# Optimization experiments

Hardware: AMD Instinct MI355X
Metric: run time of the kernel (lower is better)

The kernel has to match this reference:

```python
import jax, jax.numpy as jnp
import numpy as np

V, E, T_MAX, H, L = 20000, 384, 512, 8, 8
D = E // H  # head size 48
FF = 4 * E


def setup_inputs() -> dict:
    key = jax.random.key(0)
    ks = jax.random.split(key, 24)
    B, T = 16, 512
    s = 0.02
    return {
        "index": jax.random.randint(ks[0], (B, T), 0, V, dtype=jnp.int64),
        "targets": jax.random.randint(ks[1], (B, T), 0, V, dtype=jnp.int64),
        "tok_emb": s * jax.random.normal(ks[2], (V, E), jnp.float32),
        "pos_emb": s * jax.random.normal(ks[3], (T_MAX, E), jnp.float32),
        "Wq": s * jax.random.normal(ks[4], (L, E, H, D), jnp.float32),
        "bq": jnp.zeros((L, H, D), jnp.float32),
        "Wk": s * jax.random.normal(ks[5], (L, E, H, D), jnp.float32),
        "bk": jnp.zeros((L, H, D), jnp.float32),
        "Wv": s * jax.random.normal(ks[6], (L, E, H, D), jnp.float32),
        "bv": jnp.zeros((L, H, D), jnp.float32),
        "Wo": s * jax.random.normal(ks[7], (L, E, E), jnp.float32),
        "bo": jnp.zeros((L, E), jnp.float32),
        "ln1_g": jnp.ones((L, E), jnp.float32),
        "ln1_b": jnp.zeros((L, E), jnp.float32),
        "ln2_g": jnp.ones((L, E), jnp.float32),
        "ln2_b": jnp.zeros((L, E), jnp.float32),
        "W1": s * jax.random.normal(ks[8], (L, E, FF), jnp.float32),
        "b1": jnp.zeros((L, FF), jnp.float32),
        "W2": s * jax.random.normal(ks[9], (L, FF, E), jnp.float32),
        "b2": jnp.zeros((L, E), jnp.float32),
        "lnf_g": jnp.ones((E,), jnp.float32),
        "lnf_b": jnp.zeros((E,), jnp.float32),
        "lm_b": jnp.zeros((V,), jnp.float32),
    }


def layernorm(x, g, b, eps=1e-5):
    mu = jnp.mean(x, axis=-1, keepdims=True)
    var = jnp.var(x, axis=-1, keepdims=True)
    return (x - mu) * jax.lax.rsqrt(var + eps) * g + b


def reference(index, targets, tok_emb, pos_emb, Wq, bq, Wk, bk, Wv, bv, Wo, bo,
              ln1_g, ln1_b, ln2_g, ln2_b, W1, b1, W2, b2, lnf_g, lnf_b, lm_b):
    B, T = index.shape
    x = tok_emb[index] + pos_emb[:T]  # [B,T,E]
    causal = jnp.tril(jnp.ones((T, T), bool))
    scale = D ** -0.5
    for l in range(L):
        h = layernorm(x, ln1_g[l], ln1_b[l])
        q = jnp.einsum('bte,ehd->bthd', h, Wq[l]) + bq[l]
        k = jnp.einsum('bte,ehd->bthd', h, Wk[l]) + bk[l]
        v = jnp.einsum('bte,ehd->bthd', h, Wv[l]) + bv[l]
        scores = jnp.einsum('bqhd,bkhd->bhqk', q, k) * scale
        scores = jnp.where(causal, scores, -jnp.inf)
        w = jax.nn.softmax(scores, axis=-1)
        attn = jnp.einsum('bhqk,bkhd->bqhd', w, v).reshape(B, T, E)
        x = x + attn @ Wo[l] + bo[l]
        h2 = layernorm(x, ln2_g[l], ln2_b[l])
        ff = jax.nn.gelu(h2 @ W1[l] + b1[l], approximate=False) @ W2[l] + b2[l]
        x = x + ff
    x = layernorm(x, lnf_g, lnf_b)
    logits = x @ tok_emb.T + lm_b  # tied weights
    logits = logits.reshape(B * T, V)
    logp = jax.nn.log_softmax(logits, axis=-1)
    loss = -jnp.mean(jnp.take_along_axis(logp, targets.reshape(-1, 1), axis=-1))
    return logits, loss
```

## Files before the change

### kernel.cpp

```cpp
#include <hip/hip_runtime.h>
#include <hip/hip_bf16.h>
#include <math.h>

#define M_ROWS 8192
#define E_DIM 384
#define FF_DIM 1536
#define V_DIM 20000
#define VPAD 20096
#define N_LAYER 8
#define QK_SCALE 0.14433756729740643f
#define PSTRIDE 320
#define NPART 314

typedef __bf16 bf16x8 __attribute__((ext_vector_type(8)));
typedef short  s16x8  __attribute__((ext_vector_type(8)));
typedef float  f32x4  __attribute__((ext_vector_type(4)));
typedef __hip_bfloat16 bf16_t;

__device__ __forceinline__ void gl2lds16(const void* g, void* l) {
    __builtin_amdgcn_global_load_lds((const __attribute__((address_space(1))) void*)g,
                                     (__attribute__((address_space(3))) void*)l, 16, 0, 0);
}
__device__ __forceinline__ unsigned short bf16bits(float v) {
    return __builtin_bit_cast(unsigned short, __float2bfloat16(v));
}

__global__ __launch_bounds__(256) void tconv_kernel(
    const float* __restrict__ in, bf16_t* __restrict__ out,
    int K, int N, int outRows, int rowoff)
{
    __shared__ float tile[32][33];
    const int n0 = blockIdx.x * 32, k0 = blockIdx.y * 32;
    const float* ip = in + (size_t)blockIdx.z * K * N;
    bf16_t* op = out + (size_t)blockIdx.z * outRows * K;
    const int tx = threadIdx.x & 31, ty = threadIdx.x >> 5;
#pragma unroll
    for (int i = 0; i < 32; i += 8)
        tile[ty + i][tx] = ip[(size_t)(k0 + ty + i) * N + n0 + tx];
    __syncthreads();
#pragma unroll
    for (int i = 0; i < 32; i += 8)
        op[(size_t)(rowoff + n0 + ty + i) * K + k0 + tx] = __float2bfloat16(tile[tx][ty + i]);
}

__global__ __launch_bounds__(256) void tokconv_kernel(
    const float* __restrict__ tok, bf16_t* __restrict__ out)
{
    const int total = VPAD * 48;
    for (int idx = blockIdx.x * 256 + threadIdx.x; idx < total; idx += gridDim.x * 256) {
        int row = idx / 48, gc = idx - row * 48;
        int col = gc * 8;
        s16x8 pk = {};
        if (row < V_DIM) {
            const float* tp = tok + (size_t)row * E_DIM + col;
            float4 f0 = *(const float4*)tp;
            float4 f1 = *(const float4*)(tp + 4);
            pk[0] = (short)bf16bits(f0.x); pk[1] = (short)bf16bits(f0.y);
            pk[2] = (short)bf16bits(f0.z); pk[3] = (short)bf16bits(f0.w);
            pk[4] = (short)bf16bits(f1.x); pk[5] = (short)bf16bits(f1.y);
            pk[6] = (short)bf16bits(f1.z); pk[7] = (short)bf16bits(f1.w);
        }
        *(s16x8*)&out[(size_t)row * E_DIM + col] = pk;
    }
}

__global__ __launch_bounds__(256) void bqkv_kernel(
    const float* __restrict__ bq, const float* __restrict__ bk,
    const float* __restrict__ bv, float* __restrict__ o)
{
    int i = blockIdx.x * 256 + threadIdx.x;
    if (i < N_LAYER * 1152) {
        int l = i / 1152, c = i - l * 1152;
        float v = (c < 384) ? bq[l * 384 + c] : (c < 768) ? bk[l * 384 + c - 384] : bv[l * 384 + c - 768];
        o[i] = v;
    }
}

__global__ __launch_bounds__(256) void embed_kernel(
    const int* __restrict__ idx, const float* __restrict__ tok,
    const float* __restrict__ pos, float* __restrict__ x)
{
    int row = blockIdx.x * 4 + (threadIdx.x >> 6);
    int lane = threadIdx.x & 63;
    int t = row & 511;
    int id = idx[row];
    const float* tr = tok + (size_t)id * E_DIM;
    const float* pr = pos + (size_t)t * E_DIM;
    float* xr = x + (size_t)row * E_DIM;
#pragma unroll
    for (int i = 0; i < 6; i++) { int c = lane + i * 64; xr[c] = tr[c] + pr[c]; }
}

__global__ __launch_bounds__(256) void ln_kernel(
    const float* __restrict__ x, const float* __restrict__ g,
    const float* __restrict__ b, bf16_t* __restrict__ out)
{
    int row = blockIdx.x * 4 + (threadIdx.x >> 6);
    int lane = threadIdx.x & 63;
    const float* xr = x + (size_t)row * E_DIM;
    float vals[6];
    float s = 0.f;
#pragma unroll
    for (int i = 0; i < 6; i++) { vals[i] = xr[lane + i * 64]; s += vals[i]; }
#pragma unroll
    for (int off = 1; off < 64; off <<= 1) s += __shfl_xor(s, off);
    float mu = s * (1.f / E_DIM);
    float sq = 0.f;
#pragma unroll
    for (int i = 0; i < 6; i++) { float d = vals[i] - mu; sq += d * d; }
#pragma unroll
    for (int off = 1; off < 64; off <<= 1) sq += __shfl_xor(sq, off);
    float rstd = rsqrtf(sq * (1.f / E_DIM) + 1e-5f);
    bf16_t* orow = out + (size_t)row * E_DIM;
#pragma unroll
    for (int i = 0; i < 6; i++) {
        int c = lane + i * 64;
        orow[c] = __float2bfloat16((vals[i] - mu) * rstd * g[c] + b[c]);
    }
}

template <int MODE, int MREP>
__global__ __launch_bounds__(256) void gemm_kernel(
    const bf16_t* __restrict__ A, const bf16_t* __restrict__ Bt,
    const float* __restrict__ bias, void* __restrict__ Cv, void* __restrict__ C2,
    int Ncols, int K)
{
    constexpr int BMR = MREP * 32;
    constexpr int ASH = BMR * 32;
    constexpr int BUFSH = ASH + 4096;
    constexpr int NLD = MREP / 2 + 2;
    __shared__ __align__(16) short smem[3 * BUFSH];
    const int t = threadIdx.x;
    const int w = t >> 6, lane = t & 63;
    const int wm = w >> 1, wn = w & 1;
    const int bm = (MODE == 3 ? blockIdx.x : blockIdx.y) * BMR;
    const int bn = (MODE == 3 ? blockIdx.y : blockIdx.x) * 128;

    f32x4 acc[MREP][4];
#pragma unroll
    for (int m = 0; m < MREP; m++)
#pragma unroll
        for (int n = 0; n < 4; n++)
            acc[m][n] = (f32x4){0.f, 0.f, 0.f, 0.f};

    const int lg = lane >> 4;
    const int ll = lane & 15;
    const int nt = K / 32;

    auto stagef = [&](int kt, int buf) {
        short* sA = smem + buf * BUFSH;
        short* sB = sA + ASH;
#pragma unroll
        for (int i = 0; i < MREP / 2; i++) {
            int li = i * 256 + t;
            int g = li >> (MREP == 4 ? 7 : 6);
            int row = li & (BMR - 1);
            gl2lds16(A + (size_t)(bm + row) * K + kt + g * 8,
                     sA + (size_t)(i * 256 + w * 64) * 8);
        }
#pragma unroll
        for (int i = 0; i < 2; i++) {
            int li = i * 256 + t;
            gl2lds16(Bt + (size_t)(bn + (li & 127)) * K + kt + (li >> 7) * 8,
                     sB + (size_t)(i * 256 + w * 64) * 8);
        }
    };

    stagef(0, 0);
    stagef(32, 1);

    for (int tt = 0; tt < nt; ++tt) {
        if (tt + 2 < nt) {
            stagef((tt + 2) * 32, (tt + 2) % 3);
            asm volatile("s_waitcnt vmcnt(%0)" :: "n"(2 * NLD) : "memory");
        } else if (tt + 1 < nt) {
            asm volatile("s_waitcnt vmcnt(%0)" :: "n"(NLD) : "memory");
        } else {
            asm volatile("s_waitcnt vmcnt(0)" ::: "memory");
        }
        __builtin_amdgcn_s_barrier();

        const short* sA = smem + (tt % 3) * BUFSH;
        const short* sB = sA + ASH;
        bf16x8 af[MREP], bfr[4];
#pragma unroll
        for (int m = 0; m < MREP; m++)
            af[m] = __builtin_bit_cast(bf16x8,
                *(const s16x8*)&sA[(lg * BMR + wm * (BMR / 2) + m * 16 + ll) * 8]);
#pragma unroll
        for (int n = 0; n < 4; n++)
            bfr[n] = __builtin_bit_cast(bf16x8,
                *(const s16x8*)&sB[(lg * 128 + wn * 64 + n * 16 + ll) * 8]);
#pragma unroll
        for (int m = 0; m < MREP; m++)
#pragma unroll
            for (int n = 0; n < 4; n++)
                acc[m][n] = __builtin_amdgcn_mfma_f32_16x16x32_bf16(bfr[n], af[m], acc[m][n], 0, 0, 0);

        __builtin_amdgcn_s_barrier();
    }

    const int rowm0 = bm + wm * (BMR / 2) + ll;
    const int coln0 = bn + wn * 64 + lg * 4;

    if constexpr (MODE == 4) {
        if (bn < 768) {
            bf16_t* qkvb = (bf16_t*)Cv;
            const float sc = (bn >= 384) ? 1.f : QK_SCALE;
#pragma unroll
            for (int n = 0; n < 4; n++) {
                const int coln = coln0 + n * 16;
                const float4 b4 = *(const float4*)&bias[coln];
#pragma unroll
                for (int m = 0; m < MREP; m++) {
                    const int row = rowm0 + m * 16;
                    ushort4 pk;
                    pk.x = bf16bits((acc[m][n][0] + b4.x) * sc);
                    pk.y = bf16bits((acc[m][n][1] + b4.y) * sc);
                    pk.z = bf16bits((acc[m][n][2] + b4.z) * sc);
                    pk.w = bf16bits((acc[m][n][3] + b4.w) * sc);
                    *(ushort4*)&qkvb[(size_t)row * 1152 + coln] = pk;
                }
            }
        } else {
            bf16_t* vtb = (bf16_t*)C2;
            const int cc0 = coln0 - 768;
#pragma unroll
            for (int n = 0; n < 4; n++) {
                const float4 b4 = *(const float4*)&bias[coln0 + n * 16];
#pragma unroll
                for (int m = 0; m < MREP; m++) {
                    const int row = rowm0 + m * 16;
                    const int bb = row >> 9, tt2 = row & 511;
                    bf16_t* vb = vtb + (size_t)bb * 384 * 512 + tt2;
                    vb[(size_t)(cc0 + n * 16 + 0) * 512] = __float2bfloat16(acc[m][n][0] + b4.x);
                    vb[(size_t)(cc0 + n * 16 + 1) * 512] = __float2bfloat16(acc[m][n][1] + b4.y);
                    vb[(size_t)(cc0 + n * 16 + 2) * 512] = __float2bfloat16(acc[m][n][2] + b4.z);
                    vb[(size_t)(cc0 + n * 16 + 3) * 512] = __float2bfloat16(acc[m][n][3] + b4.w);
                }
            }
        }
    } else if constexpr (MODE == 1) {
        float* C = (float*)Cv;
#pragma unroll
        for (int n = 0; n < 4; n++) {
            const int coln = coln0 + n * 16;
            const float4 b4 = *(const float4*)&bias[coln];
#pragma unroll
            for (int m = 0; m < MREP; m++) {
                const int row = rowm0 + m * 16;
                float4 cv = *(float4*)&C[(size_t)row * Ncols + coln];
                cv.x += acc[m][n][0] + b4.x;
                cv.y += acc[m][n][1] + b4.y;
                cv.z += acc[m][n][2] + b4.z;
                cv.w += acc[m][n][3] + b4.w;
                *(float4*)&C[(size_t)row * Ncols + coln] = cv;
            }
        }
    } else if constexpr (MODE == 2) {
        bf16_t* O = (bf16_t*)Cv;
#pragma unroll
        for (int n = 0; n < 4; n++) {
            const int coln = coln0 + n * 16;
            const float4 b4 = *(const float4*)&bias[coln];
#pragma unroll
            for (int m = 0; m < MREP; m++) {
                const int row = rowm0 + m * 16;
                float v0 = acc[m][n][0] + b4.x, v1 = acc[m][n][1] + b4.y;
                float v2 = acc[m][n][2] + b4.z, v3 = acc[m][n][3] + b4.w;
                v0 = 0.5f * v0 * (1.f + erff(v0 * 0.70710678118654752f));
                v1 = 0.5f * v1 * (1.f + erff(v1 * 0.70710678118654752f));
                v2 = 0.5f * v2 * (1.f + erff(v2 * 0.70710678118654752f));
                v3 = 0.5f * v3 * (1.f + erff(v3 * 0.70710678118654752f));
                ushort4 pk;
                pk.x = bf16bits(v0); pk.y = bf16bits(v1);
                pk.z = bf16bits(v2); pk.w = bf16bits(v3);
                *(ushort4*)&O[(size_t)row * Ncols + coln] = pk;
            }
        }
    } else if constexpr (MODE == 3) {
        float* C = (float*)Cv;
        float* pbuf = (float*)C2;
        const int ptile = blockIdx.y * 2 + wn;
#pragma unroll
        for (int m = 0; m < MREP; m++) {
            const int row = rowm0 + m * 16;
            float se = 0.f;
#pragma unroll
            for (int n = 0; n < 4; n++) {
                const int coln = coln0 + n * 16;
                if (coln + 3 < Ncols) {
                    const float4 b4 = *(const float4*)&bias[coln];
                    f32x4 v;
                    v[0] = acc[m][n][0] + b4.x;
                    v[1] = acc[m][n][1] + b4.y;
                    v[2] = acc[m][n][2] + b4.z;
                    v[3] = acc[m][n][3] + b4.w;
                    __builtin_nontemporal_store(v, (f32x4*)&C[(size_t)row * Ncols + coln]);
                    se += __expf(v[0]) + __expf(v[1]) + __expf(v[2]) + __expf(v[3]);
                } else {
#pragma unroll
                    for (int e = 0; e < 4; e++) {
                        int col = coln + e;
                        if (col < Ncols) {
                            float v = acc[m][n][e] + bias[col];
                            __builtin_nontemporal_store(v, &C[(size_t)row * Ncols + col]);
                            se += __expf(v);
                        }
                    }
                }
            }
            se += __shfl_xor(se, 16);
            se += __shfl_xor(se, 32);
            if (lg == 0)
                __builtin_nontemporal_store(se, &pbuf[(size_t)row * PSTRIDE + ptile]);
        }
    }
}

__global__ __launch_bounds__(256) void attn_kernel(
    const bf16_t* __restrict__ qkvb, const bf16_t* __restrict__ vt,
    bf16_t* __restrict__ o)
{
    const int bh = blockIdx.y;
    const int b = bh >> 3, h = bh & 7;
    __shared__ unsigned short psm[4608];
    const int tid = threadIdx.x;
    const int w = tid >> 6, lane = tid & 63;
    const int ll = lane & 15, g = lane >> 4;

    const bf16_t* kptr = qkvb + (size_t)b * 512 * 1152 + 384 + h * 48;
    const bf16_t* vptr = vt + (size_t)b * 384 * 512 + (size_t)h * 48 * 512;

    auto runQ = [&](int qt) {
        const int q0 = qt * 64;
        const int q_abs = q0 + ll * 4 + w;

        const bf16_t* qrow = qkvb + (size_t)(b * 512 + q_abs) * 1152 + h * 48;
        bf16x8 qf0 = __builtin_bit_cast(bf16x8, *(const s16x8*)(qrow + g * 8));
        bf16x8 qf1 = {};
        if (g < 2) qf1 = __builtin_bit_cast(bf16x8, *(const s16x8*)(qrow + 32 + g * 8));

        f32x4 oacc[3];
#pragma unroll
        for (int df = 0; df < 3; df++) oacc[df] = (f32x4){0.f, 0.f, 0.f, 0.f};
        float ssum = 0.f;
        const int ntiles = 2 * (qt + 1);

        auto loadK = [&](int kbase, bf16x8& c00, bf16x8& c01, bf16x8& c10, bf16x8& c11) {
            const bf16_t* kr0 = kptr + (size_t)(kbase + ll) * 1152;
            const bf16_t* kr1 = kptr + (size_t)(kbase + 16 + ll) * 1152;
            c00 = __builtin_bit_cast(bf16x8, *(const s16x8*)(kr0 + g * 8));
            c10 = __builtin_bit_cast(bf16x8, *(const s16x8*)(kr1 + g * 8));
            bf16x8 z = {};
            c01 = (g < 2) ? __builtin_bit_cast(bf16x8, *(const s16x8*)(kr0 + 32 + g * 8)) : z;
            c11 = (g < 2) ? __builtin_bit_cast(bf16x8, *(const s16x8*)(kr1 + 32 + g * 8)) : z;
        };

        auto doTile = [&](int kbase, int parity,
                          const bf16x8& c00, const bf16x8& c01, const bf16x8& c10, const bf16x8& c11,
                          bool pf, int nbase,
                          bf16x8& n00, bf16x8& n01, bf16x8& n10, bf16x8& n11) {
            bf16x8 vf[3];
#pragma unroll
            for (int df = 0; df < 3; df++)
                vf[df] = __builtin_bit_cast(bf16x8,
                    *(const s16x8*)(vptr + (size_t)(df * 16 + ll) * 512 + kbase + g * 8));
            if (pf) loadK(nbase, n00, n01, n10, n11);

            f32x4 sfr[2];
            {
                f32x4 z0 = {0.f, 0.f, 0.f, 0.f};
                z0 = __builtin_amdgcn_mfma_f32_16x16x32_bf16(c00, qf0, z0, 0, 0, 0);
                z0 = __builtin_amdgcn_mfma_f32_16x16x32_bf16(c01, qf1, z0, 0, 0, 0);
                sfr[0] = z0;
                f32x4 z1 = {0.f, 0.f, 0.f, 0.f};
                z1 = __builtin_amdgcn_mfma_f32_16x16x32_bf16(c10, qf0, z1, 0, 0, 0);
                z1 = __builtin_amdgcn_mfma_f32_16x16x32_bf16(c11, qf1, z1, 0, 0, 0);
                sfr[1] = z1;
            }

            float p[8];
#pragma unroll
            for (int f = 0; f < 2; f++)
#pragma unroll
                for (int j = 0; j < 4; j++) {
                    int key = kbase + f * 16 + g * 4 + j;
                    float sv = sfr[f][j];
                    sv = (key > q_abs) ? -1e30f : sv;
                    float pv = __expf(fminf(sv, 20.f));
                    p[f * 4 + j] = pv;
                    ssum += pv;
                }

            const int pbase = (w * 2 + parity) * 576;
#pragma unroll
            for (int f = 0; f < 2; f++)
#pragma unroll
                for (int j = 0; j < 4; j++)
                    psm[pbase + (f * 16 + g * 4 + j) * 18 + ll] = bf16bits(p[f * 4 + j]);
            s16x8 pr;
#pragma unroll
            for (int i = 0; i < 8; i++)
                pr[i] = (short)psm[pbase + (g * 8 + i) * 18 + ll];
            bf16x8 pfr = __builtin_bit_cast(bf16x8, pr);
#pragma unroll
            for (int df = 0; df < 3; df++)
                oacc[df] = __builtin_amdgcn_mfma_f32_16x16x32_bf16(vf[df], pfr, oacc[df], 0, 0, 0);
        };

        bf16x8 kA0, kA1, kA2, kA3, kB0, kB1, kB2, kB3;
        loadK(0, kA0, kA1, kA2, kA3);
        for (int kt = 0; kt < ntiles; kt += 2) {
            doTile(kt * 32, 0, kA0, kA1, kA2, kA3,
                   true, (kt + 1) * 32, kB0, kB1, kB2, kB3);
            doTile((kt + 1) * 32, 1, kB0, kB1, kB2, kB3,
                   (kt + 2) < ntiles, (kt + 2) * 32, kA0, kA1, kA2, kA3);
        }

        ssum += __shfl_xor(ssum, 16);
        ssum += __shfl_xor(ssum, 32);
        float inv = 1.f / ssum;
        bf16_t* orow = o + (size_t)(b * 512 + q_abs) * 384 + h * 48;
#pragma unroll
        for (int df = 0; df < 3; df++) {
            ushort4 pk;
            pk.x = bf16bits(oacc[df][0] * inv);
            pk.y = bf16bits(oacc[df][1] * inv);
            pk.z = bf16bits(oacc[df][2] * inv);
            pk.w = bf16bits(oacc[df][3] * inv);
            *(ushort4*)&orow[df * 16 + g * 4] = pk;
        }
    };

    runQ(blockIdx.x);
    runQ(7 - blockIdx.x);
}

__global__ __launch_bounds__(256) void loss_row2_kernel(
    const float* __restrict__ pbuf, const float* __restrict__ logits,
    const int* __restrict__ targets, float* __restrict__ rowloss)
{
    int row = blockIdx.x * 4 + (threadIdx.x >> 6);
    int lane = threadIdx.x & 63;
    const float* pr = pbuf + (size_t)row * PSTRIDE;
    float s = 0.f;
    for (int i = lane; i < NPART; i += 64) s += pr[i];
#pragma unroll
    for (int off = 1; off < 64; off <<= 1) s += __shfl_xor(s, off);
    if (lane == 0) {
        int tgt = targets[row];
        rowloss[row] = logf(s) - logits[(size_t)row * V_DIM + tgt];
    }
}

__global__ __launch_bounds__(256) void loss_reduce_kernel(
    const float* __restrict__ rowloss, float* __restrict__ out)
{
    int t = threadIdx.x;
    __shared__ float red[4];
    float s = 0.f;
    for (int i = t; i < M_ROWS; i += 256) s += rowloss[i];
#pragma unroll
    for (int off = 1; off < 64; off <<= 1) s += __shfl_xor(s, off);
    if ((t & 63) == 0) red[t >> 6] = s;
    __syncthreads();
    if (t == 0) out[0] = (red[0] + red[1] + red[2] + red[3]) * (1.f / M_ROWS);
}

extern "C" void kernel_launch(void* const* d_in, const int* in_sizes, int n_in,
                              void* d_out, int out_size, void* d_ws, size_t ws_size,
                              hipStream_t stream)
{
    const int*   index   = (const int*)d_in[0];
    const int*   targets = (const int*)d_in[1];
    const float* tok_emb = (const float*)d_in[2];
    const float* pos_emb = (const float*)d_in[3];
    const float* Wq = (const float*)d_in[4];
    const float* bq = (const float*)d_in[5];
    const float* Wk = (const float*)d_in[6];
    const float* bk = (const float*)d_in[7];
    const float* Wv = (const float*)d_in[8];
    const float* bv = (const float*)d_in[9];
    const float* Wo = (const float*)d_in[10];
    const float* bo = (const float*)d_in[11];
    const float* ln1_g = (const float*)d_in[12];
    const float* ln1_b = (const float*)d_in[13];
    const float* ln2_g = (const float*)d_in[14];
    const float* ln2_b = (const float*)d_in[15];
    const float* W1 = (const float*)d_in[16];
    const float* b1 = (const float*)d_in[17];
    const float* W2 = (const float*)d_in[18];
    const float* b2 = (const float*)d_in[19];
    const float* lnf_g = (const float*)d_in[20];
    const float* lnf_b = (const float*)d_in[21];
    const float* lm_b  = (const float*)d_in[22];

    float* out = (float*)d_out;
    char* wsb = (char*)d_ws;

    float*  x     = (float*)(wsb + 0);
    bf16_t* hbuf  = (bf16_t*)(wsb + 12582912);
    bf16_t* obuf  = (bf16_t*)(wsb + 18874368);
    bf16_t* qkvb  = (bf16_t*)(wsb + 25165824);
    bf16_t* vtb   = (bf16_t*)(wsb + 44040192);
    bf16_t* ffmid = (bf16_t*)(wsb + 18874368);
    float*  pbuf  = (float*)(wsb + 25165824);
    bf16_t* tokb  = (bf16_t*)(wsb + 50331648);
    bf16_t* qkvw  = (bf16_t*)(wsb + 65765376);
    bf16_t* wo_t  = (bf16_t*)(wsb + 72843264);
    bf16_t* w1_t  = (bf16_t*)(wsb + 75202560);
    bf16_t* w2_t  = (bf16_t*)(wsb + 84639744);
    float*  bqkv  = (float*)(wsb + 94076928);
    float*  rowloss = (float*)(wsb + 94113792);

    tokconv_kernel<<<2048, 256, 0, stream>>>(tok_emb, tokb);
    tconv_kernel<<<dim3(12, 12, 8), 256, 0, stream>>>(Wq, qkvw, 384, 384, 1152, 0);
    tconv_kernel<<<dim3(12, 12, 8), 256, 0, stream>>>(Wk, qkvw, 384, 384, 1152, 384);
    tconv_kernel<<<dim3(12, 12, 8), 256, 0, stream>>>(Wv, qkvw, 384, 384, 1152, 768);
    tconv_kernel<<<dim3(12, 12, 8), 256, 0, stream>>>(Wo, wo_t, 384, 384, 384, 0);
    tconv_kernel<<<dim3(48, 12, 8), 256, 0, stream>>>(W1, w1_t, 384, 1536, 1536, 0);
    tconv_kernel<<<dim3(12, 48, 8), 256, 0, stream>>>(W2, w2_t, 1536, 384, 384, 0);
    bqkv_kernel<<<36, 256, 0, stream>>>(bq, bk, bv, bqkv);

    embed_kernel<<<2048, 256, 0, stream>>>(index, tok_emb, pos_emb, x);

    for (int l = 0; l < N_LAYER; l++) {
        const bf16_t* qkvw_l = qkvw + (size_t)l * 1152 * 384;
        const float*  bqkv_l = bqkv + l * 1152;
        ln_kernel<<<2048, 256, 0, stream>>>(x, ln1_g + l * E_DIM, ln1_b + l * E_DIM, hbuf);
        gemm_kernel<4, 4><<<dim3(9, 64), 256, 0, stream>>>(
            hbuf, qkvw_l, bqkv_l, qkvb, vtb, 1152, 384);
        attn_kernel<<<dim3(4, 128), 256, 0, stream>>>(qkvb, vtb, obuf);
        gemm_kernel<1, 2><<<dim3(3, 128), 256, 0, stream>>>(
            obuf, wo_t + (size_t)l * 384 * 384, bo + l * E_DIM, x, nullptr, 384, 384);
        ln_kernel<<<2048, 256, 0, stream>>>(x, ln2_g + l * E_DIM, ln2_b + l * E_DIM, hbuf);
        gemm_kernel<2, 4><<<dim3(12, 64), 256, 0, stream>>>(
            hbuf, w1_t + (size_t)l * 1536 * 384, b1 + l * FF_DIM, ffmid, nullptr, 1536, 384);
        gemm_kernel<1, 2><<<dim3(3, 128), 256, 0, stream>>>(
            ffmid, w2_t + (size_t)l * 384 * 1536, b2 + l * E_DIM, x, nullptr, 384, 1536);
    }

    ln_kernel<<<2048, 256, 0, stream>>>(x, lnf_g, lnf_b, hbuf);
    gemm_kernel<3, 4><<<dim3(64, 157), 256, 0, stream>>>(
        hbuf, tokb, lm_b, out, pbuf, V_DIM, 384);

    loss_row2_kernel<<<2048, 256, 0, stream>>>(pbuf, out, targets, rowloss);
    loss_reduce_kernel<<<1, 256, 0, stream>>>(rowloss, out + (size_t)M_ROWS * V_DIM);
}
```

Before: 1.684 ms.

## Add dedicated logits kernel with register-resident A rows and streamed vocab tiles

Replaces the generic MODE 3 GEMM for the LM head with a persistent-style kernel. Each block keeps its 128 rows of normalized activations in registers for the full K=384 and loops over a range of 128-wide vocab tiles, triple-buffering only the B tiles in LDS. The grid shrinks from 64x157 to 64x8 blocks, and partial sum-exp entries drop to one per 128-column tile. This is meant to cut repeated A loads and per-block launch overhead for the logits GEMM, at the cost of heavy register use (24 bf16x8 A fragments plus 16 accumulators) and only 512 blocks, which may limit occupancy and latency hiding.

Result: faster. 1.641 ms (median of 2 runs) (-2.6%).

```diff
diff --git a/kernel.cpp b/kernel.cpp
--- a/kernel.cpp
+++ b/kernel.cpp
@@ -9,8 +9,8 @@
 #define VPAD 20096
 #define N_LAYER 8
 #define QK_SCALE 0.14433756729740643f
-#define PSTRIDE 320
-#define NPART 314
+#define PSTRIDE 160
+#define NPART 157
 
 typedef __bf16 bf16x8 __attribute__((ext_vector_type(8)));
 typedef short  s16x8  __attribute__((ext_vector_type(8)));
@@ -133,8 +133,8 @@
     const int t = threadIdx.x;
     const int w = t >> 6, lane = t & 63;
     const int wm = w >> 1, wn = w & 1;
-    const int bm = (MODE == 3 ? blockIdx.x : blockIdx.y) * BMR;
-    const int bn = (MODE == 3 ? blockIdx.y : blockIdx.x) * 128;
+    const int bm = blockIdx.y * BMR;
+    const int bn = blockIdx.x * 128;
 
     f32x4 acc[MREP][4];
 #pragma unroll
@@ -278,33 +278,108 @@
                 *(ushort4*)&O[(size_t)row * Ncols + coln] = pk;
             }
         }
-    } else if constexpr (MODE == 3) {
-        float* C = (float*)Cv;
-        float* pbuf = (float*)C2;
-        const int ptile = blockIdx.y * 2 + wn;
-#pragma unroll
-        for (int m = 0; m < MREP; m++) {
-            const int row = rowm0 + m * 16;
+    }
+}
+
+__global__ __launch_bounds__(256) void logits_kernel(
+    const bf16_t* __restrict__ A, const bf16_t* __restrict__ Bt,
+    const float* __restrict__ bias, float* __restrict__ C,
+    float* __restrict__ pbuf)
+{
+    __shared__ __align__(16) short smem[3 * 4096];
+    const int t = threadIdx.x;
+    const int w = t >> 6, lane = t & 63;
+    const int lg = lane >> 4, ll = lane & 15;
+    const int bm = blockIdx.x * 128;
+    const int wr = bm + w * 32;
+    const int tstart = (blockIdx.y * 157) >> 3;
+    const int tend = ((blockIdx.y + 1) * 157) >> 3;
+
+    bf16x8 af[12][2];
+#pragma unroll
+    for (int kt = 0; kt < 12; kt++)
+#pragma unroll
+        for (int m = 0; m < 2; m++)
+            af[kt][m] = __builtin_bit_cast(bf16x8,
+                *(const s16x8*)(A + (size_t)(wr + m * 16 + ll) * E_DIM + kt * 32 + lg * 8));
+
+    auto stageB = [&](int tile, int kt, int buf) {
+        short* sB = smem + buf * 4096;
+#pragma unroll
+        for (int i = 0; i < 2; i++) {
+            int li = i * 256 + t;
+            gl2lds16(Bt + (size_t)(tile * 128 + (li & 127)) * E_DIM + kt * 32 + (li >> 7) * 8,
+                     sB + (size_t)(i * 256 + w * 64) * 8);
+        }
+    };
+
+    stageB(tstart, 0, 0);
+    stageB(tstart, 1, 1);
+
+    for (int tile = tstart; tile < tend; ++tile) {
+        f32x4 acc[2][8];
+#pragma unroll
+        for (int m = 0; m < 2; m++)
+#pragma unroll
+            for (int n = 0; n < 8; n++)
+                acc[m][n] = (f32x4){0.f, 0.f, 0.f, 0.f};
+
+#pragma unroll
+        for (int kt = 0; kt < 12; ++kt) {
+            const int sleft = (tend - 1 - tile) * 12 + (11 - kt);
+            if (kt + 2 < 12) {
+                stageB(tile, kt + 2, (kt + 2) % 3);
+                asm volatile("s_waitcnt vmcnt(4)" ::: "memory");
+            } else if (tile + 1 < tend) {
+                stageB(tile + 1, kt + 2 - 12, (kt + 2) % 3);
+                asm volatile("s_waitcnt vmcnt(4)" ::: "memory");
+            } else if (sleft >= 1) {
+                asm volatile("s_waitcnt vmcnt(2)" ::: "memory");
+            } else {
+                asm volatile("s_waitcnt vmcnt(0)" ::: "memory");
+            }
+            __builtin_amdgcn_s_barrier();
+
+            const short* sB = smem + (kt % 3) * 4096;
+            bf16x8 bfr[8];
+#pragma unroll
+            for (int n = 0; n < 8; n++)
+                bfr[n] = __builtin_bit_cast(bf16x8,
+                    *(const s16x8*)&sB[(lg * 128 + n * 16 + ll) * 8]);
+#pragma unroll
+            for (int m = 0; m < 2; m++)
+#pragma unroll
+                for (int n = 0; n < 8; n++)
+                    acc[m][n] = __builtin_amdgcn_mfma_f32_16x16x32_bf16(
+                        bfr[n], af[kt][m], acc[m][n], 0, 0, 0);
+
+            __builtin_amdgcn_s_barrier();
+        }
+
+        const int tc = tile * 128;
+#pragma unroll
+        for (int m = 0; m < 2; m++) {
+            const int row = wr + m * 16 + ll;
             float se = 0.f;
 #pragma unroll
-            for (int n = 0; n < 4; n++) {
-                const int coln = coln0 + n * 16;
-                if (coln + 3 < Ncols) {
+            for (int n = 0; n < 8; n++) {
+                const int coln = tc + n * 16 + lg * 4;
+                if (coln + 3 < V_DIM) {
                     const float4 b4 = *(const float4*)&bias[coln];
                     f32x4 v;
                     v[0] = acc[m][n][0] + b4.x;
                     v[1] = acc[m][n][1] + b4.y;
                     v[2] = acc[m][n][2] + b4.z;
                     v[3] = acc[m][n][3] + b4.w;
-                    __builtin_nontemporal_store(v, (f32x4*)&C[(size_t)row * Ncols + coln]);
+                    __builtin_nontemporal_store(v, (f32x4*)&C[(size_t)row * V_DIM + coln]);
                     se += __expf(v[0]) + __expf(v[1]) + __expf(v[2]) + __expf(v[3]);
                 } else {
 #pragma unroll
                     for (int e = 0; e < 4; e++) {
                         int col = coln + e;
-                        if (col < Ncols) {
+                        if (col < V_DIM) {
                             float v = acc[m][n][e] + bias[col];
-                            __builtin_nontemporal_store(v, &C[(size_t)row * Ncols + col]);
+                            __builtin_nontemporal_store(v, &C[(size_t)row * V_DIM + col]);
                             se += __expf(v);
                         }
                     }
@@ -313,7 +388,7 @@
             se += __shfl_xor(se, 16);
             se += __shfl_xor(se, 32);
             if (lg == 0)
-                __builtin_nontemporal_store(se, &pbuf[(size_t)row * PSTRIDE + ptile]);
+                __builtin_nontemporal_store(se, &pbuf[(size_t)row * PSTRIDE + tile]);
         }
     }
 }
@@ -542,8 +617,7 @@
     }
 
     ln_kernel<<<2048, 256, 0, stream>>>(x, lnf_g, lnf_b, hbuf);
-    gemm_kernel<3, 4><<<dim3(64, 157), 256, 0, stream>>>(
-        hbuf, tokb, lm_b, out, pbuf, V_DIM, 384);
+    logits_kernel<<<dim3(64, 8), 256, 0, stream>>>(hbuf, tokb, lm_b, out, pbuf);
 
     loss_row2_kernel<<<2048, 256, 0, stream>>>(pbuf, out, targets, rowloss);
     loss_reduce_kernel<<<1, 256, 0, stream>>>(rowloss, out + (size_t)M_ROWS * V_DIM);
```
